# Performance work log

Measured on AMD Instinct MI355X. Metric: run time of the kernel, lower is better.

The kernel has to match this reference:

```python
import jax, jax.numpy as jnp
import numpy as np
import math

B, H, S, D = 4, 16, 1024, 64
NEG = -1000000000.0

def setup_inputs() -> dict:
    key = jax.random.key(0)
    ks = jax.random.split(key, 6)
    return {
        "query": jax.random.normal(ks[0], (B, H, S, D), dtype=jnp.float32),
        "key": jax.random.normal(ks[1], (B, H, S, D), dtype=jnp.float32),
        "value": jax.random.normal(ks[2], (B, H, S, D), dtype=jnp.float32),
        "head_nums": H,
        "mask": jax.random.randint(ks[3], (B, S), 0, 2, dtype=jnp.int32),
        "topic_query": jax.random.normal(ks[4], (B, S, D), dtype=jnp.float32),
        "topic_key": jax.random.normal(ks[5], (B, S, D), dtype=jnp.float32),
    }

def reference(query, key, value, head_nums, mask, topic_query, topic_key):
    d = query.shape[-1]
    # scores: [B,H,S,S]
    scores = jnp.einsum("bhqd,bhkd->bhqk", query, key) / math.sqrt(d)
    # pairwise mask: [B,S,S] (mask_i * mask_j)
    pair_mask = (mask[:, :, None] * mask[:, None, :]) != 0
    scores = jnp.where(pair_mask[:, None, :, :], scores, NEG)
    # topic modulation: per-token (no head dim), broadcast over heads
    dt = topic_query.shape[-1]
    topic_scores = jnp.einsum("bqd,bkd->bqk", topic_query, topic_key) / math.sqrt(dt)
    topic_scores = jnp.where(pair_mask, topic_scores, 1.0)[:, None, :, :]  # [B,1,S,S]
    topic_probs = jax.nn.softmax(topic_scores, axis=-1)
    scores = scores * topic_probs
    p_attn = jax.nn.softmax(scores, axis=-1)
    out = jnp.einsum("bhqk,bhkd->bhqd", p_attn, value)
    return (out, p_attn)
```

## Files before the change

kernel.cpp:

```cpp
#include <hip/hip_runtime.h>

#define B_ 4
#define H_ 16
#define S_ 1024
#define D_ 64
#define NEGV -1000000000.0f

typedef __bf16 bf16x8 __attribute__((ext_vector_type(8)));
typedef __bf16 bf16x4 __attribute__((ext_vector_type(4)));
typedef float f32x4 __attribute__((ext_vector_type(4)));

#define MFMA16(A, B, C) __builtin_amdgcn_mfma_f32_16x16x32_bf16(A, B, C, 0, 0, 0)

__device__ __forceinline__ void bar_lds() {
  asm volatile("s_waitcnt lgkmcnt(0)" ::: "memory");
  __builtin_amdgcn_sched_barrier(0);
  __builtin_amdgcn_s_barrier();
  __builtin_amdgcn_sched_barrier(0);
}

__device__ __forceinline__ bf16x8 cvt8(const float* p) {
  float4 x = *(const float4*)p;
  float4 y = *(const float4*)(p + 4);
  bf16x8 f;
  f[0]=(__bf16)x.x; f[1]=(__bf16)x.y; f[2]=(__bf16)x.z; f[3]=(__bf16)x.w;
  f[4]=(__bf16)y.x; f[5]=(__bf16)y.y; f[6]=(__bf16)y.z; f[7]=(__bf16)y.w;
  return f;
}

__global__ __launch_bounds__(256) void prep_kernel(
    const float* __restrict__ K, const float* __restrict__ V,
    __bf16* __restrict__ Kb, __bf16* __restrict__ Vt)
{
  int bid = blockIdx.x;
  int sc = bid & 15;
  int bh = bid >> 4;
  int tid = threadIdx.x;
  __shared__ float s_v[64][65];

  const float* Kc = K + ((size_t)bh*S_ + sc*64)*D_;
  const float* Vc = V + ((size_t)bh*S_ + sc*64)*D_;
  __bf16* Kbc = Kb + ((size_t)bh*S_ + sc*64)*D_;

  {
    const float4* src = (const float4*)Kc + tid*4;
    float4 a = src[0], b = src[1], c = src[2], d = src[3];
    bf16x8 o0, o1;
    o0[0]=(__bf16)a.x; o0[1]=(__bf16)a.y; o0[2]=(__bf16)a.z; o0[3]=(__bf16)a.w;
    o0[4]=(__bf16)b.x; o0[5]=(__bf16)b.y; o0[6]=(__bf16)b.z; o0[7]=(__bf16)b.w;
    o1[0]=(__bf16)c.x; o1[1]=(__bf16)c.y; o1[2]=(__bf16)c.z; o1[3]=(__bf16)c.w;
    o1[4]=(__bf16)d.x; o1[5]=(__bf16)d.y; o1[6]=(__bf16)d.z; o1[7]=(__bf16)d.w;
    *(bf16x8*)(Kbc + tid*16)     = o0;
    *(bf16x8*)(Kbc + tid*16 + 8) = o1;
  }
  for (int i = tid; i < 64*16; i += 256) {
    int r = i >> 4, c4 = i & 15;
    float4 v = ((const float4*)(Vc + (size_t)r*D_))[c4];
    s_v[r][c4*4+0] = v.x; s_v[r][c4*4+1] = v.y;
    s_v[r][c4*4+2] = v.z; s_v[r][c4*4+3] = v.w;
  }
  __syncthreads();
  {
    int d = tid >> 2, seg = tid & 3;
    bf16x8 o0, o1;
    #pragma unroll
    for (int j = 0; j < 8; ++j) o0[j] = (__bf16)s_v[seg*16 + j][d];
    #pragma unroll
    for (int j = 0; j < 8; ++j) o1[j] = (__bf16)s_v[seg*16 + 8 + j][d];
    __bf16* dst = Vt + ((size_t)bh*D_ + d)*S_ + sc*64 + seg*16;
    *(bf16x8*)dst = o0;
    *(bf16x8*)(dst + 8) = o1;
  }
}

__global__ __launch_bounds__(256) void topic_kernel(
    const float* __restrict__ tq, const float* __restrict__ tk,
    const int* __restrict__ mask, __bf16* __restrict__ tp)
{
  int bid0 = blockIdx.x;
  int bid = (bid0 & 7)*32 + (bid0 >> 3);
  int qt = bid & 63, b = bid >> 6;
  int tid = threadIdx.x, wave = tid >> 6, lane = tid & 63;
  int l15 = lane & 15, lhi = lane >> 4;
  __shared__ float2 s_red[4][16];
  __shared__ __align__(16) char s_mem[4*8704];

  const int* mb = mask + b*S_;
  bf16x8 qf[2];
  #pragma unroll
  for (int dc = 0; dc < 2; ++dc)
    qf[dc] = cvt8(tq + ((size_t)b*S_ + qt*16 + l15)*D_ + dc*32 + lhi*8);
  int mq = mb[qt*16 + l15];

  f32x4 sc[16];
  #pragma unroll
  for (int kt = 0; kt < 16; ++kt) {
    int kb = wave*256 + kt*16;
    const float* kr = tk + ((size_t)b*S_ + kb + l15)*D_ + lhi*8;
    bf16x8 k0 = cvt8(kr);
    bf16x8 k1 = cvt8(kr + 32);
    f32x4 acc = {0.f,0.f,0.f,0.f};
    acc = MFMA16(k0, qf[0], acc);
    acc = MFMA16(k1, qf[1], acc);
    int4 mk = *(const int4*)(mb + kb + lhi*4);
    sc[kt][0] = (mq && mk.x) ? acc[0]*0.125f : 1.0f;
    sc[kt][1] = (mq && mk.y) ? acc[1]*0.125f : 1.0f;
    sc[kt][2] = (mq && mk.z) ? acc[2]*0.125f : 1.0f;
    sc[kt][3] = (mq && mk.w) ? acc[3]*0.125f : 1.0f;
  }
  float m = -3.4e38f;
  #pragma unroll
  for (int kt = 0; kt < 16; ++kt)
    #pragma unroll
    for (int i = 0; i < 4; ++i) m = fmaxf(m, sc[kt][i]);
  m = fmaxf(m, __shfl_xor(m, 16));
  m = fmaxf(m, __shfl_xor(m, 32));
  float sum = 0.f;
  #pragma unroll
  for (int kt = 0; kt < 16; ++kt)
    #pragma unroll
    for (int i = 0; i < 4; ++i) { sc[kt][i] = __expf(sc[kt][i] - m); sum += sc[kt][i]; }
  sum += __shfl_xor(sum, 16);
  sum += __shfl_xor(sum, 32);
  if (lane < 16) s_red[wave][l15] = make_float2(m, sum);
  bar_lds();
  float M = -3.4e38f;
  #pragma unroll
  for (int w = 0; w < 4; ++w) M = fmaxf(M, s_red[w][l15].x);
  float Z = 0.f;
  #pragma unroll
  for (int w = 0; w < 4; ++w) Z += s_red[w][l15].y * __expf(s_red[w][l15].x - M);
  float scale = __expf(m - M) / Z;

  #pragma unroll
  for (int kt = 0; kt < 16; ++kt) {
    int kb = wave*256 + kt*16;
    int4 mk = *(const int4*)(mb + kb + lhi*4);
    sc[kt][0] *= scale; if (!(mq && mk.x)) sc[kt][0] = -sc[kt][0];
    sc[kt][1] *= scale; if (!(mq && mk.y)) sc[kt][1] = -sc[kt][1];
    sc[kt][2] *= scale; if (!(mq && mk.z)) sc[kt][2] = -sc[kt][2];
    sc[kt][3] *= scale; if (!(mq && mk.w)) sc[kt][3] = -sc[kt][3];
  }

  float* xw = (float*)s_mem + wave*2176;
  __bf16* tpw = tp + ((size_t)b*S_ + qt*16)*S_ + wave*256;
  #pragma unroll
  for (int h = 0; h < 2; ++h) {
    #pragma unroll
    for (int j = 0; j < 8; ++j)
      *(f32x4*)(xw + l15*136 + j*16 + lhi*4) = sc[h*8 + j];
    bar_lds();
    #pragma unroll
    for (int rr = 0; rr < 8; ++rr) {
      int r = rr*2 + (lane >> 5);
      f32x4 a = *(f32x4*)(xw + r*136 + (lane & 31)*4);
      bf16x4 o;
      o[0]=(__bf16)a[0]; o[1]=(__bf16)a[1]; o[2]=(__bf16)a[2]; o[3]=(__bf16)a[3];
      *(bf16x4*)(tpw + (size_t)r*S_ + h*128 + (lane & 31)*4) = o;
    }
    bar_lds();
  }
}

__global__ __launch_bounds__(256) void attn_kernel(
    const float* __restrict__ Q, const __bf16* __restrict__ Kb,
    const __bf16* __restrict__ Vt, const __bf16* __restrict__ tp,
    float* __restrict__ out, float* __restrict__ pa)
{
  int bid0 = blockIdx.x;
  int bid = (bid0 & 7)*512 + (bid0 >> 3);
  int qt = bid & 63;
  int h  = (bid >> 6) & 15;
  int b  = bid >> 10;
  int tid = threadIdx.x, wave = tid >> 6, lane = tid & 63;
  int l15 = lane & 15, lhi = lane >> 4;

  __shared__ __align__(16) char s_mem[4*8704];
  __shared__ float2 s_red[4][16];

  size_t bh = (size_t)b*H_ + h;
  const __bf16* Kbh = Kb + bh*S_*D_;
  const __bf16* tpb = tp + ((size_t)b*S_ + qt*16 + l15)*S_;

  bf16x8 qf[2];
  #pragma unroll
  for (int dc = 0; dc < 2; ++dc)
    qf[dc] = cvt8(Q + (bh*S_ + qt*16 + l15)*D_ + dc*32 + lhi*8);

  f32x4 sc[16];
  bf16x8 rk0[3], rk1[3];
  bf16x4 rt[3];
  #pragma unroll
  for (int p = 0; p < 2; ++p) {
    int kb = wave*256 + p*16;
    const __bf16* kr = Kbh + (size_t)(kb + l15)*D_ + lhi*8;
    rk0[p] = *(const bf16x8*)kr;
    rk1[p] = *(const bf16x8*)(kr + 32);
    rt[p]  = *(const bf16x4*)(tpb + kb + lhi*4);
  }
  #pragma unroll
  for (int kt = 0; kt < 16; ++kt) {
    const int cur = kt % 3;
    if (kt + 2 < 16) {
      const int nxt = (kt + 2) % 3;
      int kb = wave*256 + (kt+2)*16;
      const __bf16* kr = Kbh + (size_t)(kb + l15)*D_ + lhi*8;
      rk0[nxt] = *(const bf16x8*)kr;
      rk1[nxt] = *(const bf16x8*)(kr + 32);
      rt[nxt]  = *(const bf16x4*)(tpb + kb + lhi*4);
    }
    f32x4 acc = {0.f,0.f,0.f,0.f};
    acc = MFMA16(rk0[cur], qf[0], acc);
    acc = MFMA16(rk1[cur], qf[1], acc);
    #pragma unroll
    for (int i = 0; i < 4; ++i) {
      float t = (float)rt[cur][i];
      sc[kt][i] = (t > 0.f) ? acc[i]*0.125f*t : NEGV*(-t);
    }
  }

  float m = -3.4e38f;
  #pragma unroll
  for (int kt = 0; kt < 16; ++kt)
    #pragma unroll
    for (int i = 0; i < 4; ++i) m = fmaxf(m, sc[kt][i]);
  m = fmaxf(m, __shfl_xor(m, 16));
  m = fmaxf(m, __shfl_xor(m, 32));
  float sum = 0.f;
  #pragma unroll
  for (int kt = 0; kt < 16; ++kt)
    #pragma unroll
    for (int i = 0; i < 4; ++i) { sc[kt][i] = __expf(sc[kt][i] - m); sum += sc[kt][i]; }
  sum += __shfl_xor(sum, 16);
  sum += __shfl_xor(sum, 32);
  if (lane < 16) s_red[wave][l15] = make_float2(m, sum);
  bar_lds();
  float M = -3.4e38f;
  #pragma unroll
  for (int w = 0; w < 4; ++w) M = fmaxf(M, s_red[w][l15].x);
  float Z = 0.f;
  #pragma unroll
  for (int w = 0; w < 4; ++w) Z += s_red[w][l15].y * __expf(s_red[w][l15].x - M);
  float scale = __expf(m - M) / Z;

  #pragma unroll
  for (int kt = 0; kt < 16; ++kt)
    #pragma unroll
    for (int i = 0; i < 4; ++i) sc[kt][i] *= scale;

  float* xw = (float*)s_mem + wave*2176;
  float* paw = pa + (bh*S_ + qt*16)*S_ + wave*256;
  #pragma unroll
  for (int hh = 0; hh < 2; ++hh) {
    #pragma unroll
    for (int j = 0; j < 8; ++j)
      *(f32x4*)(xw + l15*136 + j*16 + lhi*4) = sc[hh*8 + j];
    bar_lds();
    #pragma unroll
    for (int rr = 0; rr < 8; ++rr) {
      int r = rr*2 + (lane >> 5);
      f32x4 a = *(f32x4*)(xw + r*136 + (lane & 31)*4);
      __builtin_nontemporal_store(a, (f32x4*)(paw + (size_t)r*S_ + hh*128 + (lane & 31)*4));
    }
    bar_lds();
  }

  #pragma unroll
  for (int kt = 0; kt < 16; ++kt) {
    bf16x4 pb;
    pb[0] = (__bf16)sc[kt][0]; pb[1] = (__bf16)sc[kt][1];
    pb[2] = (__bf16)sc[kt][2]; pb[3] = (__bf16)sc[kt][3];
    *(bf16x4*)(s_mem + l15*2048 + ((wave*512 + kt*32 + lhi*8) ^ ((l15 & 7) << 4))) = pb;
  }
  bar_lds();

  const __bf16* Vh = Vt + (bh*D_ + wave*16 + l15)*S_ + lhi*8;
  bf16x8 rv[3];
  #pragma unroll
  for (int p = 0; p < 2; ++p) rv[p] = *(const bf16x8*)(Vh + p*32);
  f32x4 oacc = {0.f,0.f,0.f,0.f};
  #pragma unroll
  for (int ks = 0; ks < 32; ++ks) {
    if (ks + 2 < 32) rv[(ks+2)%3] = *(const bf16x8*)(Vh + (ks+2)*32);
    bf16x8 a = *(const bf16x8*)(s_mem + l15*2048 + ((ks*64 + lhi*16) ^ ((l15 & 7) << 4)));
    oacc = MFMA16(a, rv[ks%3], oacc);
  }
  #pragma unroll
  for (int i = 0; i < 4; ++i)
    __builtin_nontemporal_store(oacc[i], out + (bh*S_ + qt*16 + lhi*4 + i)*D_ + wave*16 + l15);
}

extern "C" void kernel_launch(void* const* d_in, const int* in_sizes, int n_in,
                              void* d_out, int out_size, void* d_ws, size_t ws_size,
                              hipStream_t stream) {
  const float* Q    = (const float*)d_in[0];
  const float* K    = (const float*)d_in[1];
  const float* V    = (const float*)d_in[2];
  const int*   mask = (const int*)d_in[4];
  const float* tq   = (const float*)d_in[5];
  const float* tk   = (const float*)d_in[6];

  __bf16* tp = (__bf16*)d_ws;
  __bf16* Kb = tp + (size_t)B_*S_*S_;
  __bf16* Vt = Kb + (size_t)B_*H_*S_*D_;

  float* outp = (float*)d_out;
  float* pa   = outp + (size_t)B_*H_*S_*D_;

  prep_kernel <<<B_*H_*16, 256, 0, stream>>>(K, V, Kb, Vt);
  topic_kernel<<<B_*64,    256, 0, stream>>>(tq, tk, mask, tp);
  attn_kernel <<<B_*H_*64, 256, 0, stream>>>(Q, Kb, Vt, tp, outp, pa);
}
```

Before: 192.6 us.

## Store pre-softmax scores as bf16 and halve LDS footprint for occupancy

Keeps the masked and modulated scores in bf16 registers instead of fp32, and recomputes the exponentials when writing p_attn and the PV operand. LDS use is halved by writing p_attn in four smaller tiles and staging the P matrix for PV in two halves, with V loaded directly without a prefetch ring. The K prefetch depth is cut from a triple to a double buffer. The aim is fewer VGPRs and less LDS so more blocks fit per CU. In exchange it adds extra exp work, extra barriers, and bf16 rounding of scores before softmax, which lowers p_attn accuracy.

```diff
diff --git a/kernel.cpp b/kernel.cpp
--- a/kernel.cpp
+++ b/kernel.cpp
@@ -175,7 +175,7 @@
   int tid = threadIdx.x, wave = tid >> 6, lane = tid & 63;
   int l15 = lane & 15, lhi = lane >> 4;
 
-  __shared__ __align__(16) char s_mem[4*8704];
+  __shared__ __align__(16) char s_mem[17408];
   __shared__ float2 s_red[4][16];
 
   size_t bh = (size_t)b*H_ + h;
@@ -187,23 +187,21 @@
   for (int dc = 0; dc < 2; ++dc)
     qf[dc] = cvt8(Q + (bh*S_ + qt*16 + l15)*D_ + dc*32 + lhi*8);
 
-  f32x4 sc[16];
-  bf16x8 rk0[3], rk1[3];
-  bf16x4 rt[3];
-  #pragma unroll
-  for (int p = 0; p < 2; ++p) {
-    int kb = wave*256 + p*16;
-    const __bf16* kr = Kbh + (size_t)(kb + l15)*D_ + lhi*8;
-    rk0[p] = *(const bf16x8*)kr;
-    rk1[p] = *(const bf16x8*)(kr + 32);
-    rt[p]  = *(const bf16x4*)(tpb + kb + lhi*4);
+  bf16x4 sb[16];
+  bf16x8 rk0[2], rk1[2];
+  bf16x4 rt[2];
+  {
+    const __bf16* kr = Kbh + (size_t)(wave*256 + l15)*D_ + lhi*8;
+    rk0[0] = *(const bf16x8*)kr;
+    rk1[0] = *(const bf16x8*)(kr + 32);
+    rt[0]  = *(const bf16x4*)(tpb + wave*256 + lhi*4);
   }
   #pragma unroll
   for (int kt = 0; kt < 16; ++kt) {
-    const int cur = kt % 3;
-    if (kt + 2 < 16) {
-      const int nxt = (kt + 2) % 3;
-      int kb = wave*256 + (kt+2)*16;
+    const int cur = kt & 1;
+    if (kt < 15) {
+      const int nxt = cur ^ 1;
+      int kb = wave*256 + (kt+1)*16;
       const __bf16* kr = Kbh + (size_t)(kb + l15)*D_ + lhi*8;
       rk0[nxt] = *(const bf16x8*)kr;
       rk1[nxt] = *(const bf16x8*)(kr + 32);
@@ -215,7 +213,8 @@
     #pragma unroll
     for (int i = 0; i < 4; ++i) {
       float t = (float)rt[cur][i];
-      sc[kt][i] = (t > 0.f) ? acc[i]*0.125f*t : NEGV*(-t);
+      float s = (t > 0.f) ? acc[i]*0.125f*t : NEGV*(-t);
+      sb[kt][i] = (__bf16)s;
     }
   }
 
@@ -223,14 +222,14 @@
   #pragma unroll
   for (int kt = 0; kt < 16; ++kt)
     #pragma unroll
-    for (int i = 0; i < 4; ++i) m = fmaxf(m, sc[kt][i]);
+    for (int i = 0; i < 4; ++i) m = fmaxf(m, (float)sb[kt][i]);
   m = fmaxf(m, __shfl_xor(m, 16));
   m = fmaxf(m, __shfl_xor(m, 32));
   float sum = 0.f;
   #pragma unroll
   for (int kt = 0; kt < 16; ++kt)
     #pragma unroll
-    for (int i = 0; i < 4; ++i) { sc[kt][i] = __expf(sc[kt][i] - m); sum += sc[kt][i]; }
+    for (int i = 0; i < 4; ++i) sum += __expf((float)sb[kt][i] - m);
   sum += __shfl_xor(sum, 16);
   sum += __shfl_xor(sum, 32);
   if (lane < 16) s_red[wave][l15] = make_float2(m, sum);
@@ -241,49 +240,54 @@
   float Z = 0.f;
   #pragma unroll
   for (int w = 0; w < 4; ++w) Z += s_red[w][l15].y * __expf(s_red[w][l15].x - M);
-  float scale = __expf(m - M) / Z;
-
-  #pragma unroll
-  for (int kt = 0; kt < 16; ++kt)
-    #pragma unroll
-    for (int i = 0; i < 4; ++i) sc[kt][i] *= scale;
-
-  float* xw = (float*)s_mem + wave*2176;
+  const float scale = __expf(m - M) / Z;
+  bar_lds();
+
+  float* xw = (float*)s_mem + wave*4352/4;
   float* paw = pa + (bh*S_ + qt*16)*S_ + wave*256;
   #pragma unroll
-  for (int hh = 0; hh < 2; ++hh) {
-    #pragma unroll
-    for (int j = 0; j < 8; ++j)
-      *(f32x4*)(xw + l15*136 + j*16 + lhi*4) = sc[hh*8 + j];
-    bar_lds();
-    #pragma unroll
-    for (int rr = 0; rr < 8; ++rr) {
-      int r = rr*2 + (lane >> 5);
-      f32x4 a = *(f32x4*)(xw + r*136 + (lane & 31)*4);
-      __builtin_nontemporal_store(a, (f32x4*)(paw + (size_t)r*S_ + hh*128 + (lane & 31)*4));
-    }
-    bar_lds();
-  }
-
-  #pragma unroll
-  for (int kt = 0; kt < 16; ++kt) {
-    bf16x4 pb;
-    pb[0] = (__bf16)sc[kt][0]; pb[1] = (__bf16)sc[kt][1];
-    pb[2] = (__bf16)sc[kt][2]; pb[3] = (__bf16)sc[kt][3];
-    *(bf16x4*)(s_mem + l15*2048 + ((wave*512 + kt*32 + lhi*8) ^ ((l15 & 7) << 4))) = pb;
-  }
-  bar_lds();
+  for (int hh = 0; hh < 4; ++hh) {
+    #pragma unroll
+    for (int j = 0; j < 4; ++j) {
+      int kt = hh*4 + j;
+      f32x4 pv;
+      #pragma unroll
+      for (int i = 0; i < 4; ++i) pv[i] = __expf((float)sb[kt][i] - m) * scale;
+      *(f32x4*)(xw + l15*68 + j*16 + lhi*4) = pv;
+    }
+    bar_lds();
+    #pragma unroll
+    for (int rr = 0; rr < 4; ++rr) {
+      int r = rr*4 + lhi;
+      f32x4 a = *(f32x4*)(xw + r*68 + l15*4);
+      __builtin_nontemporal_store(a, (f32x4*)(paw + (size_t)r*S_ + hh*64 + l15*4));
+    }
+    bar_lds();
+  }
 
   const __bf16* Vh = Vt + (bh*D_ + wave*16 + l15)*S_ + lhi*8;
-  bf16x8 rv[3];
-  #pragma unroll
-  for (int p = 0; p < 2; ++p) rv[p] = *(const bf16x8*)(Vh + p*32);
   f32x4 oacc = {0.f,0.f,0.f,0.f};
   #pragma unroll
-  for (int ks = 0; ks < 32; ++ks) {
-    if (ks + 2 < 32) rv[(ks+2)%3] = *(const bf16x8*)(Vh + (ks+2)*32);
-    bf16x8 a = *(const bf16x8*)(s_mem + l15*2048 + ((ks*64 + lhi*16) ^ ((l15 & 7) << 4)));
-    oacc = MFMA16(a, rv[ks%3], oacc);
+  for (int h2 = 0; h2 < 2; ++h2) {
+    if ((wave >> 1) == h2) {
+      int cb = (wave & 1)*256;
+      #pragma unroll
+      for (int kt = 0; kt < 16; ++kt) {
+        bf16x4 pb;
+        #pragma unroll
+        for (int i = 0; i < 4; ++i) pb[i] = (__bf16)(__expf((float)sb[kt][i] - m) * scale);
+        int col = cb + kt*16 + lhi*4;
+        *(bf16x4*)(s_mem + l15*1024 + ((col*2) ^ ((l15 & 7) << 4))) = pb;
+      }
+    }
+    bar_lds();
+    #pragma unroll
+    for (int ks = 0; ks < 16; ++ks) {
+      bf16x8 a  = *(const bf16x8*)(s_mem + l15*1024 + ((ks*64 + lhi*16) ^ ((l15 & 7) << 4)));
+      bf16x8 bv = *(const bf16x8*)(Vh + h2*512 + ks*32);
+      oacc = MFMA16(a, bv, oacc);
+    }
+    bar_lds();
   }
   #pragma unroll
   for (int i = 0; i < 4; ++i)
```

After: 189.9 us. About the same (-1.4%).

## Stage raw scores in LDS as bf16 and do row-wise softmax per wave

Applied to the files above, without the earlier changes.

Scores are no longer held in registers across the whole key range. Each wave writes its masked, topic-scaled scores as bf16 into a swizzled LDS tile, and the softmax then runs per row, with each wave handling four rows via wave-wide shuffles. Normalized probabilities are written straight to global memory and back into LDS for the PV MFMA. Software prefetching of K/V, the cross-wave max/sum merge, vectorized coalesced p_attn stores and nontemporal stores are removed. The intent is to cut register pressure and cross-wave reduction, but pre-softmax scores are now rounded to bf16, which changes the p_attn values, and memory traffic uses scalar loads and stores.

```diff
diff --git a/kernel.cpp b/kernel.cpp
--- a/kernel.cpp
+++ b/kernel.cpp
@@ -175,119 +175,75 @@
   int tid = threadIdx.x, wave = tid >> 6, lane = tid & 63;
   int l15 = lane & 15, lhi = lane >> 4;
 
-  __shared__ __align__(16) char s_mem[4*8704];
-  __shared__ float2 s_red[4][16];
+  __shared__ __align__(16) char s_p[16*2048];
 
   size_t bh = (size_t)b*H_ + h;
   const __bf16* Kbh = Kb + bh*S_*D_;
-  const __bf16* tpb = tp + ((size_t)b*S_ + qt*16 + l15)*S_;
+  const __bf16* tpb = tp + ((size_t)b*S_ + qt*16)*S_;
 
   bf16x8 qf[2];
   #pragma unroll
   for (int dc = 0; dc < 2; ++dc)
     qf[dc] = cvt8(Q + (bh*S_ + qt*16 + l15)*D_ + dc*32 + lhi*8);
 
-  f32x4 sc[16];
-  bf16x8 rk0[3], rk1[3];
-  bf16x4 rt[3];
-  #pragma unroll
-  for (int p = 0; p < 2; ++p) {
-    int kb = wave*256 + p*16;
-    const __bf16* kr = Kbh + (size_t)(kb + l15)*D_ + lhi*8;
-    rk0[p] = *(const bf16x8*)kr;
-    rk1[p] = *(const bf16x8*)(kr + 32);
-    rt[p]  = *(const bf16x4*)(tpb + kb + lhi*4);
-  }
-  #pragma unroll
   for (int kt = 0; kt < 16; ++kt) {
-    const int cur = kt % 3;
-    if (kt + 2 < 16) {
-      const int nxt = (kt + 2) % 3;
-      int kb = wave*256 + (kt+2)*16;
-      const __bf16* kr = Kbh + (size_t)(kb + l15)*D_ + lhi*8;
-      rk0[nxt] = *(const bf16x8*)kr;
-      rk1[nxt] = *(const bf16x8*)(kr + 32);
-      rt[nxt]  = *(const bf16x4*)(tpb + kb + lhi*4);
-    }
+    int kb = wave*256 + kt*16;
+    int kcol = kb + l15;
+    const __bf16* kr = Kbh + (size_t)kcol*D_ + lhi*8;
+    bf16x8 k0 = *(const bf16x8*)kr;
+    bf16x8 k1 = *(const bf16x8*)(kr + 32);
     f32x4 acc = {0.f,0.f,0.f,0.f};
-    acc = MFMA16(rk0[cur], qf[0], acc);
-    acc = MFMA16(rk1[cur], qf[1], acc);
+    acc = MFMA16(qf[0], k0, acc);
+    acc = MFMA16(qf[1], k1, acc);
     #pragma unroll
     for (int i = 0; i < 4; ++i) {
-      float t = (float)rt[cur][i];
-      sc[kt][i] = (t > 0.f) ? acc[i]*0.125f*t : NEGV*(-t);
-    }
-  }
-
-  float m = -3.4e38f;
-  #pragma unroll
-  for (int kt = 0; kt < 16; ++kt)
-    #pragma unroll
-    for (int i = 0; i < 4; ++i) m = fmaxf(m, sc[kt][i]);
-  m = fmaxf(m, __shfl_xor(m, 16));
-  m = fmaxf(m, __shfl_xor(m, 32));
-  float sum = 0.f;
-  #pragma unroll
-  for (int kt = 0; kt < 16; ++kt)
-    #pragma unroll
-    for (int i = 0; i < 4; ++i) { sc[kt][i] = __expf(sc[kt][i] - m); sum += sc[kt][i]; }
-  sum += __shfl_xor(sum, 16);
-  sum += __shfl_xor(sum, 32);
-  if (lane < 16) s_red[wave][l15] = make_float2(m, sum);
+      int row = lhi*4 + i;
+      float t = (float)tpb[(size_t)row*S_ + kcol];
+      float s = (t > 0.f) ? acc[i]*0.125f*t : NEGV*(-t);
+      *(__bf16*)(s_p + row*2048 + ((kcol*2) ^ ((row&7)<<4))) = (__bf16)s;
+    }
+  }
   bar_lds();
-  float M = -3.4e38f;
-  #pragma unroll
-  for (int w = 0; w < 4; ++w) M = fmaxf(M, s_red[w][l15].x);
-  float Z = 0.f;
-  #pragma unroll
-  for (int w = 0; w < 4; ++w) Z += s_red[w][l15].y * __expf(s_red[w][l15].x - M);
-  float scale = __expf(m - M) / Z;
-
-  #pragma unroll
-  for (int kt = 0; kt < 16; ++kt)
-    #pragma unroll
-    for (int i = 0; i < 4; ++i) sc[kt][i] *= scale;
-
-  float* xw = (float*)s_mem + wave*2176;
-  float* paw = pa + (bh*S_ + qt*16)*S_ + wave*256;
-  #pragma unroll
-  for (int hh = 0; hh < 2; ++hh) {
-    #pragma unroll
-    for (int j = 0; j < 8; ++j)
-      *(f32x4*)(xw + l15*136 + j*16 + lhi*4) = sc[hh*8 + j];
-    bar_lds();
-    #pragma unroll
-    for (int rr = 0; rr < 8; ++rr) {
-      int r = rr*2 + (lane >> 5);
-      f32x4 a = *(f32x4*)(xw + r*136 + (lane & 31)*4);
-      __builtin_nontemporal_store(a, (f32x4*)(paw + (size_t)r*S_ + hh*128 + (lane & 31)*4));
-    }
-    bar_lds();
-  }
-
-  #pragma unroll
-  for (int kt = 0; kt < 16; ++kt) {
-    bf16x4 pb;
-    pb[0] = (__bf16)sc[kt][0]; pb[1] = (__bf16)sc[kt][1];
-    pb[2] = (__bf16)sc[kt][2]; pb[3] = (__bf16)sc[kt][3];
-    *(bf16x4*)(s_mem + l15*2048 + ((wave*512 + kt*32 + lhi*8) ^ ((l15 & 7) << 4))) = pb;
+
+  #pragma unroll
+  for (int r = 0; r < 4; ++r) {
+    int row = wave*4 + r;
+    int swz = (row & 7) << 4;
+    float sv[16]; float m = -3.4e38f;
+    #pragma unroll
+    for (int j = 0; j < 16; ++j) {
+      sv[j] = (float)*(const __bf16*)(s_p + row*2048 + (((lane + j*64)*2) ^ swz));
+      m = fmaxf(m, sv[j]);
+    }
+    #pragma unroll
+    for (int o = 32; o >= 1; o >>= 1) m = fmaxf(m, __shfl_xor(m, o));
+    float ev[16]; float sum = 0.f;
+    #pragma unroll
+    for (int j = 0; j < 16; ++j) { ev[j] = __expf(sv[j]-m); sum += ev[j]; }
+    #pragma unroll
+    for (int o = 32; o >= 1; o >>= 1) sum += __shfl_xor(sum, o);
+    float inv = 1.0f/sum;
+    float* par = pa + (bh*S_ + qt*16 + row)*S_;
+    #pragma unroll
+    for (int j = 0; j < 16; ++j) {
+      float pv = ev[j]*inv;
+      par[lane + j*64] = pv;
+      *(__bf16*)(s_p + row*2048 + (((lane + j*64)*2) ^ swz)) = (__bf16)pv;
+    }
   }
   bar_lds();
 
   const __bf16* Vh = Vt + (bh*D_ + wave*16 + l15)*S_ + lhi*8;
-  bf16x8 rv[3];
-  #pragma unroll
-  for (int p = 0; p < 2; ++p) rv[p] = *(const bf16x8*)(Vh + p*32);
   f32x4 oacc = {0.f,0.f,0.f,0.f};
-  #pragma unroll
+  #pragma unroll 8
   for (int ks = 0; ks < 32; ++ks) {
-    if (ks + 2 < 32) rv[(ks+2)%3] = *(const bf16x8*)(Vh + (ks+2)*32);
-    bf16x8 a = *(const bf16x8*)(s_mem + l15*2048 + ((ks*64 + lhi*16) ^ ((l15 & 7) << 4)));
-    oacc = MFMA16(a, rv[ks%3], oacc);
+    bf16x8 a  = *(const bf16x8*)(s_p + l15*2048 + ((ks*64 + lhi*16) ^ ((l15 & 7) << 4)));
+    bf16x8 bv = *(const bf16x8*)(Vh + ks*32);
+    oacc = MFMA16(a, bv, oacc);
   }
   #pragma unroll
   for (int i = 0; i < 4; ++i)
-    __builtin_nontemporal_store(oacc[i], out + (bh*S_ + qt*16 + lhi*4 + i)*D_ + wave*16 + l15);
+    out[(bh*S_ + qt*16 + lhi*4 + i)*D_ + wave*16 + l15] = oacc[i];
 }
 
 extern "C" void kernel_launch(void* const* d_in, const int* in_sizes, int n_in,
```

Measured after the change: 182.8 us (median of 2 runs). 1.05x faster.
